# Kernel optimization log

Hardware: AMD Instinct MI355X
Metric: run time of the kernel (lower is better)

Reference implementation:

```python
import jax, jax.numpy as jnp
import numpy as np

N_EXPERTS = 8
TOP_K = 2


def setup_inputs() -> dict:
    key = jax.random.key(0)
    ks = jax.random.split(key, 5)
    B, T, D, E, H = 4, 2048, 1024, N_EXPERTS, 2730  # H = int(2*D*4/3)
    x = jax.random.normal(ks[0], (B, T, D), dtype=jnp.float32)
    gate_w = jax.random.normal(ks[1], (E, D), dtype=jnp.float32) * 0.02
    w1 = jax.random.normal(ks[2], (E, H, D), dtype=jnp.float32) * 0.02
    w3 = jax.random.normal(ks[3], (E, H, D), dtype=jnp.float32) * 0.02
    w2 = jax.random.normal(ks[4], (E, D, H), dtype=jnp.float32) * 0.02
    return {"x": x, "gate_w": gate_w, "w1": w1, "w3": w3, "w2": w2}


def reference(x, gate_w, w1, w3, w2):
    B, T, D = x.shape
    E = gate_w.shape[0]
    x_flat = x.reshape(-1, D)  # [N, D], N = B*T
    N = x_flat.shape[0]

    # Router: top-k over softmax probabilities, renormalized over selected experts
    logits = x_flat @ gate_w.T                      # [N, E]
    probs = jax.nn.softmax(logits, axis=-1)         # [N, E]
    top_v, top_i = jax.lax.top_k(probs, TOP_K)      # [N, K]
    top_v = top_v / jnp.sum(top_v, axis=-1, keepdims=True)

    # Dense combine weights [N, E]: weight of expert e for each token (0 if not selected).
    # top_k indices are distinct per token, so scatter-add equals scatter-set here.
    combine = jnp.zeros((N, E), dtype=x.dtype).at[
        jnp.arange(N)[:, None], top_i
    ].add(top_v)

    # Weighted combine of SwiGLU experts (loop over small fixed expert count).
    out = jnp.zeros_like(x_flat)
    for e in range(E):
        gate = jax.nn.silu(x_flat @ w1[e].T)        # [N, H]
        up = x_flat @ w3[e].T                       # [N, H]
        y = (gate * up) @ w2[e].T                   # [N, D]
        out = out + combine[:, e:e + 1] * y

    aux_loss = jnp.asarray(0.0, dtype=x.dtype)  # use_aux_loss=False / eval mode
    return out.reshape(B, T, D), aux_loss
```

## Files before the change

### kernel.cpp

```cpp
#include <hip/hip_runtime.h>
#include <hip/hip_bf16.h>

#define N_TOK 8192
#define D_DIM 1024
#define E_NUM 8
#define H_DIM 2730
#define HP    2816
#define NP    5632
#define NROWS (N_TOK*2)
#define MAXTILES 136
#define MAXT256  72

typedef __bf16 bf16;
typedef __bf16 bf16x8 __attribute__((ext_vector_type(8)));
typedef __bf16 bf16x4 __attribute__((ext_vector_type(4)));
typedef float  f32x4  __attribute__((ext_vector_type(4)));

__device__ __forceinline__ void gload_lds16(const bf16* g, bf16* l) {
  __builtin_amdgcn_global_load_lds((const __attribute__((address_space(1))) void*)g,
                                   (__attribute__((address_space(3))) void*)l, 16, 0, 0);
}
#define VMCNT(n) asm volatile("s_waitcnt vmcnt(" #n ")" ::: "memory")
#define LGKM0()  asm volatile("s_waitcnt lgkmcnt(0)" ::: "memory")
#define BAR() __builtin_amdgcn_s_barrier()

__global__ void conv13_kernel(const float* __restrict__ w1, const float* __restrict__ w3,
                              bf16* __restrict__ Bp) {
  int i = blockIdx.x * blockDim.x + threadIdx.x;
  if (i >= E_NUM * NP * 128) return;
  int c8 = i & 127;
  int r  = (i >> 7) % NP;
  int e  = i / (NP * 128);
  int hc = ((r >> 5) << 4) + (r & 15);
  bf16x8 o;
  if (hc < H_DIM) {
    const float* s = (((r >> 4) & 1) ? w3 : w1) + ((long)e * H_DIM + hc) * D_DIM + c8 * 8;
    float4 a0 = ((const float4*)s)[0], a1 = ((const float4*)s)[1];
    o[0]=(bf16)a0.x; o[1]=(bf16)a0.y; o[2]=(bf16)a0.z; o[3]=(bf16)a0.w;
    o[4]=(bf16)a1.x; o[5]=(bf16)a1.y; o[6]=(bf16)a1.z; o[7]=(bf16)a1.w;
  } else {
    #pragma unroll
    for (int j = 0; j < 8; j++) o[j] = (bf16)0.f;
  }
  ((bf16x8*)Bp)[i] = o;
}

__global__ void conv_w2_kernel(const float* __restrict__ src, bf16* __restrict__ dst) {
  int i = blockIdx.x * blockDim.x + threadIdx.x;
  if (i >= E_NUM * D_DIM * (HP / 8)) return;
  int c8 = i % (HP / 8);
  int row = i / (HP / 8);
  int c = c8 * 8;
  const float* s = src + (long)row * H_DIM + c;
  bf16x8 o;
  #pragma unroll
  for (int j = 0; j < 8; j++) o[j] = (c + j < H_DIM) ? (bf16)s[j] : (bf16)0.f;
  ((bf16x8*)dst)[i] = o;
}

__global__ void router_kernel(const float* __restrict__ x, const float* __restrict__ gw,
                              int* __restrict__ topi, float* __restrict__ topw,
                              int* __restrict__ counts) {
  int t = blockIdx.x * (blockDim.x >> 6) + (threadIdx.x >> 6);
  int lane = threadIdx.x & 63;
  if (t >= N_TOK) return;
  const float* xr = x + (long)t * D_DIM;
  float acc[E_NUM];
  #pragma unroll
  for (int e = 0; e < E_NUM; e++) acc[e] = 0.f;
  for (int j = 0; j < D_DIM / 64; j++) {
    float xv = xr[j * 64 + lane];
    #pragma unroll
    for (int e = 0; e < E_NUM; e++) acc[e] += xv * gw[e * D_DIM + j * 64 + lane];
  }
  #pragma unroll
  for (int e = 0; e < E_NUM; e++) {
    float v = acc[e];
    #pragma unroll
    for (int s = 32; s > 0; s >>= 1) v += __shfl_xor(v, s, 64);
    acc[e] = v;
  }
  if (lane == 0) {
    int b0 = -1, b1 = -1; float v0 = -1e30f, v1 = -1e30f;
    #pragma unroll
    for (int e = 0; e < E_NUM; e++) {
      float v = acc[e];
      if (v > v0) { v1 = v0; b1 = b0; v0 = v; b0 = e; }
      else if (v > v1) { v1 = v; b1 = e; }
    }
    float w0 = 1.f / (1.f + expf(v1 - v0));
    topi[t * 2] = b0; topi[t * 2 + 1] = b1;
    topw[t * 2] = w0; topw[t * 2 + 1] = 1.f - w0;
    atomicAdd(&counts[b0], 1); atomicAdd(&counts[b1], 1);
  }
}

__global__ void tiles_kernel(const int* __restrict__ counts, int* __restrict__ offs,
                             int* __restrict__ tlist, int* __restrict__ tlist2) {
  __shared__ int so[E_NUM + 1], sb[E_NUM + 1], sb2[E_NUM + 1];
  int t = threadIdx.x;
  if (t == 0) {
    int s = 0, b = 0, b2 = 0;
    for (int e = 0; e < E_NUM; e++) {
      so[e] = s; sb[e] = b; sb2[e] = b2;
      int ne = counts[e];
      s += ne; b += (ne + 127) >> 7; b2 += (ne + 255) >> 8;
    }
    so[E_NUM] = s; sb[E_NUM] = b; sb2[E_NUM] = b2;
  }
  __syncthreads();
  if (t <= E_NUM) offs[t] = so[t];
  for (int i = t; i < MAXTILES; i += blockDim.x) {
    int v = -1;
    #pragma unroll
    for (int e = 0; e < E_NUM; e++)
      if (i >= sb[e] && i < sb[e + 1]) v = (e << 8) | (i - sb[e]);
    tlist[i] = v;
  }
  for (int i = t; i < MAXT256; i += blockDim.x) {
    int v = -1;
    #pragma unroll
    for (int e = 0; e < E_NUM; e++)
      if (i >= sb2[e] && i < sb2[e + 1]) v = (e << 8) | (i - sb2[e]);
    tlist2[i] = v;
  }
}

__global__ void scatter_kernel(const int* __restrict__ topi, const float* __restrict__ topw,
                               const int* __restrict__ offs, int* __restrict__ cursor,
                               int* __restrict__ rowmap, float* __restrict__ roww,
                               int* __restrict__ rowoftok) {
  __shared__ int hist[E_NUM], base[E_NUM];
  int i = blockIdx.x * blockDim.x + threadIdx.x;
  if (threadIdx.x < E_NUM) hist[threadIdx.x] = 0;
  __syncthreads();
  int e = 0, lpos = 0;
  bool act = (i < NROWS);
  if (act) { e = topi[i]; lpos = atomicAdd(&hist[e], 1); }
  __syncthreads();
  if (threadIdx.x < E_NUM) base[threadIdx.x] = atomicAdd(&cursor[threadIdx.x], hist[threadIdx.x]);
  __syncthreads();
  if (act) {
    int row = offs[e] + base[e] + lpos;
    rowmap[row] = i >> 1;
    roww[row] = topw[i];
    rowoftok[i] = row;
  }
}

__global__ void gather_kernel(const float* __restrict__ x, const int* __restrict__ rowmap,
                              bf16* __restrict__ Xg) {
  int r = blockIdx.x * (blockDim.x >> 6) + (threadIdx.x >> 6);
  int lane = threadIdx.x & 63;
  if (r >= NROWS) return;
  int t = rowmap[r];
  const float4* src = (const float4*)(x + (long)t * D_DIM);
  bf16x4* dst = (bf16x4*)(Xg + (long)r * D_DIM);
  #pragma unroll
  for (int j = 0; j < 4; j++) {
    float4 v = src[j * 64 + lane];
    bf16x4 o; o[0]=(bf16)v.x; o[1]=(bf16)v.y; o[2]=(bf16)v.z; o[3]=(bf16)v.w;
    dst[j * 64 + lane] = o;
  }
}

__global__ void combine_kernel(const bf16* __restrict__ y0p, const bf16* __restrict__ y1p,
                               const int* __restrict__ rowoftok,
                               const float* __restrict__ topw, float* __restrict__ out) {
  int t = blockIdx.x * (blockDim.x >> 6) + (threadIdx.x >> 6);
  int lane = threadIdx.x & 63;
  if (t >= N_TOK) return;
  int r0 = rowoftok[t * 2], r1 = rowoftok[t * 2 + 1];
  float w0 = topw[t * 2], w1 = topw[t * 2 + 1];
  const bf16x8* a0 = (const bf16x8*)(y0p + (long)r0 * D_DIM);
  const bf16x8* a1 = (const bf16x8*)(y1p + (long)r0 * D_DIM);
  const bf16x8* b0 = (const bf16x8*)(y0p + (long)r1 * D_DIM);
  const bf16x8* b1 = (const bf16x8*)(y1p + (long)r1 * D_DIM);
  float* o = out + (long)t * D_DIM;
  #pragma unroll
  for (int j = 0; j < 2; j++) {
    int idx = j * 64 + lane;
    bf16x8 va0 = a0[idx], va1 = a1[idx], vb0 = b0[idx], vb1 = b1[idx];
    float4 v0, v1;
    v0.x = w0*((float)va0[0]+(float)va1[0]) + w1*((float)vb0[0]+(float)vb1[0]);
    v0.y = w0*((float)va0[1]+(float)va1[1]) + w1*((float)vb0[1]+(float)vb1[1]);
    v0.z = w0*((float)va0[2]+(float)va1[2]) + w1*((float)vb0[2]+(float)vb1[2]);
    v0.w = w0*((float)va0[3]+(float)va1[3]) + w1*((float)vb0[3]+(float)vb1[3]);
    v1.x = w0*((float)va0[4]+(float)va1[4]) + w1*((float)vb0[4]+(float)vb1[4]);
    v1.y = w0*((float)va0[5]+(float)va1[5]) + w1*((float)vb0[5]+(float)vb1[5]);
    v1.z = w0*((float)va0[6]+(float)va1[6]) + w1*((float)vb0[6]+(float)vb1[6]);
    v1.w = w0*((float)va0[7]+(float)va1[7]) + w1*((float)vb0[7]+(float)vb1[7]);
    float4* op = (float4*)(o + idx * 8);
    op[0] = v0; op[1] = v1;
  }
}


#define G1_STAGE(SB, T) do { \
    _Pragma("unroll") for (int L_ = 0; L_ < 4; L_++) \
      gload_lds16(aS[L_] + (T) * 32, smem + (SB) + w * 2048 + L_ * 512); \
    _Pragma("unroll") for (int L_ = 0; L_ < 2; L_++) \
      gload_lds16(bS[L_] + (T) * 32, smem + (SB) + 8192 + w * 1024 + L_ * 512); \
  } while (0)

#define G1_READ0(SB) do { \
    _Pragma("unroll") for (int m_ = 0; m_ < 4; m_++) \
      af[m_] = *(const bf16x8*)&smem[(SB) + (w * 64 + m_ * 16 + fr) * 32 + qp]; \
    _Pragma("unroll") for (int q_ = 0; q_ < 4; q_++) \
      bf0[q_] = *(const bf16x8*)&smem[(SB) + 8192 + (q_ * 16 + fr) * 32 + qp]; \
  } while (0)

#define G1_MFMA0() do { __builtin_amdgcn_s_setprio(1); \
    _Pragma("unroll") for (int m_ = 0; m_ < 4; m_++) \
    _Pragma("unroll") for (int q_ = 0; q_ < 4; q_++) \
      acc[m_][q_] = __builtin_amdgcn_mfma_f32_16x16x32_bf16(af[m_], bf0[q_], acc[m_][q_], 0, 0, 0); \
    __builtin_amdgcn_s_setprio(0); } while (0)

#define G1_READ1(SB) do { \
    _Pragma("unroll") for (int q_ = 0; q_ < 4; q_++) \
      bf1[q_] = *(const bf16x8*)&smem[(SB) + 8192 + ((q_ + 4) * 16 + fr) * 32 + qp]; \
  } while (0)

#define G1_MFMA1() do { __builtin_amdgcn_s_setprio(1); \
    _Pragma("unroll") for (int m_ = 0; m_ < 4; m_++) \
    _Pragma("unroll") for (int q_ = 0; q_ < 4; q_++) \
      acc[m_][q_ + 4] = __builtin_amdgcn_mfma_f32_16x16x32_bf16(af[m_], bf1[q_], acc[m_][q_ + 4], 0, 0, 0); \
    __builtin_amdgcn_s_setprio(0); } while (0)

__global__ __launch_bounds__(256, 2) void gemm1_kernel(
    const bf16* __restrict__ Xg, const bf16* __restrict__ Bp,
    const int* __restrict__ counts, const int* __restrict__ offs,
    const int* __restrict__ tlist2, bf16* __restrict__ h) {
  int bid = blockIdx.x;
  int tile = bid / 44, col = bid - tile * 44;
  int te = tlist2[tile];
  if (te < 0) return;
  int e = te >> 8, tm = te & 255;
  int ne = counts[e];
  int row_base = offs[e];
  int n0 = col * 128;

  __shared__ bf16 smem[3 * 12288];
  int tid = threadIdx.x, w = tid >> 6, lane = tid & 63;
  int fr = lane & 15, hi = lane >> 4;
  int qp = (hi ^ ((fr >> 1) & 3)) * 8;
  int srcq = ((lane & 3) ^ ((lane >> 3) & 3)) * 8;
  int srow = lane >> 2;

  f32x4 acc[4][8];
  #pragma unroll
  for (int m = 0; m < 4; m++)
    #pragma unroll
    for (int q = 0; q < 8; q++) acc[m][q] = (f32x4)0.f;

  const bf16* Bpe = Bp + (long)e * NP * D_DIM;
  const bf16* aS[4];
  const bf16* bS[2];
  #pragma unroll
  for (int L = 0; L < 4; L++) {
    int ra = row_base + min(tm * 256 + w * 64 + L * 16 + srow, ne - 1);
    aS[L] = Xg + (long)ra * D_DIM + srcq;
  }
  #pragma unroll
  for (int L = 0; L < 2; L++) {
    int rb = n0 + w * 32 + L * 16 + srow;
    bS[L] = Bpe + (long)rb * D_DIM + srcq;
  }

  bf16x8 af[4], bf0[4], bf1[4];

  G1_STAGE(0, 0); G1_STAGE(12288, 1);
  VMCNT(6); BAR();

  int sbC = 0, sbS = 24576;
  for (int t = 0; t < 30; t++) {
    G1_READ0(sbC);
    G1_STAGE(sbS, t + 2);
    BAR();
    G1_MFMA0();
    G1_READ1(sbC);
    G1_MFMA1();
    LGKM0(); VMCNT(6); BAR();
    sbC += 12288; if (sbC > 24576) sbC = 0;
    sbS += 12288; if (sbS > 24576) sbS = 0;
  }
  { G1_READ0(sbC); BAR(); G1_MFMA0(); G1_READ1(sbC); G1_MFMA1(); LGKM0(); VMCNT(0); BAR();
    sbC += 12288; if (sbC > 24576) sbC = 0; }
  { G1_READ0(sbC); G1_MFMA0(); G1_READ1(sbC); G1_MFMA1(); }

  int crow4 = hi * 4;
  #pragma unroll
  for (int m = 0; m < 4; m++)
    #pragma unroll
    for (int j = 0; j < 4; j++) {
      int rloc = tm * 256 + w * 64 + m * 16 + crow4 + j;
      if (rloc < ne) {
        long hrow = (long)(row_base + rloc) * HP;
        #pragma unroll
        for (int p = 0; p < 4; p++) {
          int col2 = (n0 >> 1) + p * 16 + fr;
          float g = acc[m][2 * p][j], u = acc[m][2 * p + 1][j];
          h[hrow + col2] = (bf16)((g / (1.f + __expf(-g))) * u);
        }
      }
    }
}

#define G2_STAGE(SB, T) do { \
    _Pragma("unroll") for (int L_ = 0; L_ < 2; L_++) \
      gload_lds16(aS[L_] + (T) * 32, smem2 + (SB) + w * 1024 + L_ * 512); \
    _Pragma("unroll") for (int L_ = 0; L_ < 4; L_++) \
      gload_lds16(bS[L_] + (T) * 32, smem2 + (SB) + 4096 + (L_ * 4 + w) * 512); \
  } while (0)

#define G2_READ0(SB) do { \
    _Pragma("unroll") for (int m_ = 0; m_ < 4; m_++) \
      af[m_] = *(const bf16x8*)&smem2[(SB) + (wr * 64 + m_ * 16 + fr) * 32 + qp]; \
    _Pragma("unroll") for (int n_ = 0; n_ < 4; n_++) \
      bf0[n_] = *(const bf16x8*)&smem2[(SB) + 4096 + (wc * 128 + n_ * 16 + fr) * 32 + qp]; \
  } while (0)

#define G2_MFMA0() do { __builtin_amdgcn_s_setprio(1); \
    _Pragma("unroll") for (int m_ = 0; m_ < 4; m_++) \
    _Pragma("unroll") for (int n_ = 0; n_ < 4; n_++) \
      acc[m_][n_] = __builtin_amdgcn_mfma_f32_16x16x32_bf16(af[m_], bf0[n_], acc[m_][n_], 0, 0, 0); \
    __builtin_amdgcn_s_setprio(0); } while (0)

#define G2_READ1(SB) do { \
    _Pragma("unroll") for (int n_ = 0; n_ < 4; n_++) \
      bf1[n_] = *(const bf16x8*)&smem2[(SB) + 4096 + (wc * 128 + (n_ + 4) * 16 + fr) * 32 + qp]; \
  } while (0)

#define G2_MFMA1() do { __builtin_amdgcn_s_setprio(1); \
    _Pragma("unroll") for (int m_ = 0; m_ < 4; m_++) \
    _Pragma("unroll") for (int n_ = 0; n_ < 4; n_++) \
      acc[m_][n_ + 4] = __builtin_amdgcn_mfma_f32_16x16x32_bf16(af[m_], bf1[n_], acc[m_][n_ + 4], 0, 0, 0); \
    __builtin_amdgcn_s_setprio(0); } while (0)

__global__ __launch_bounds__(256, 2) void gemm2_kernel(
    const bf16* __restrict__ h, const bf16* __restrict__ w2b,
    const int* __restrict__ counts, const int* __restrict__ offs,
    const int* __restrict__ tlist, bf16* __restrict__ y0p, bf16* __restrict__ y1p) {
  int bid = blockIdx.x;
  int tile = bid >> 3, col = (bid >> 1) & 3, ks = bid & 1;
  int te = tlist[tile];
  if (te < 0) return;
  int e = te >> 8, tm = te & 255;
  int ne = counts[e];
  int row_base = offs[e];
  int n0 = col * 256;
  int k0 = ks * 1408;

  __shared__ bf16 smem2[3 * 12288];
  int tid = threadIdx.x, w = tid >> 6, lane = tid & 63;
  int wr = w >> 1, wc = w & 1;
  int fr = lane & 15, hi = lane >> 4;
  int qp = (hi ^ ((fr >> 1) & 3)) * 8;
  int srcq = ((lane & 3) ^ ((lane >> 3) & 3)) * 8;
  int srow = lane >> 2;

  f32x4 acc[4][8];
  #pragma unroll
  for (int m = 0; m < 4; m++)
    #pragma unroll
    for (int n = 0; n < 8; n++) acc[m][n] = (f32x4)0.f;

  const bf16* w2e = w2b + (long)e * D_DIM * HP;
  const bf16* aS[2];
  const bf16* bS[4];
  #pragma unroll
  for (int L = 0; L < 2; L++) {
    int ra = row_base + min(tm * 128 + w * 32 + L * 16 + srow, ne - 1);
    aS[L] = h + (long)ra * HP + k0 + srcq;
  }
  #pragma unroll
  for (int L = 0; L < 4; L++) {
    int rb = n0 + (L * 4 + w) * 16 + srow;
    bS[L] = w2e + (long)rb * HP + k0 + srcq;
  }

  bf16x8 af[4], bf0[4], bf1[4];

  G2_STAGE(0, 0); G2_STAGE(12288, 1);
  VMCNT(6); BAR();

  int sbC = 0, sbS = 24576;
  for (int t = 0; t < 42; t++) {
    G2_READ0(sbC);
    G2_STAGE(sbS, t + 2);
    BAR();
    G2_MFMA0();
    G2_READ1(sbC);
    G2_MFMA1();
    LGKM0(); VMCNT(6); BAR();
    sbC += 12288; if (sbC > 24576) sbC = 0;
    sbS += 12288; if (sbS > 24576) sbS = 0;
  }
  { G2_READ0(sbC); BAR(); G2_MFMA0(); G2_READ1(sbC); G2_MFMA1(); LGKM0(); VMCNT(0); BAR();
    sbC += 12288; if (sbC > 24576) sbC = 0; }
  { G2_READ0(sbC); G2_MFMA0(); G2_READ1(sbC); G2_MFMA1(); }

  bf16* y = ks ? y1p : y0p;
  int crow4 = hi * 4;
  #pragma unroll
  for (int m = 0; m < 4; m++)
    #pragma unroll
    for (int j = 0; j < 4; j++) {
      int rloc = tm * 128 + wr * 64 + m * 16 + crow4 + j;
      if (rloc < ne) {
        long yrow = (long)(row_base + rloc) * D_DIM;
        #pragma unroll
        for (int n = 0; n < 8; n++) {
          int col2 = n0 + wc * 128 + n * 16 + fr;
          y[yrow + col2] = (bf16)acc[m][n][j];
        }
      }
    }
}

extern "C" void kernel_launch(void* const* d_in, const int* in_sizes, int n_in,
                              void* d_out, int out_size, void* d_ws, size_t ws_size,
                              hipStream_t stream) {
  const float* x  = (const float*)d_in[0];
  const float* gw = (const float*)d_in[1];
  const float* w1 = (const float*)d_in[2];
  const float* w3 = (const float*)d_in[3];
  const float* w2 = (const float*)d_in[4];
  float* out = (float*)d_out;

  char* ws = (char*)d_ws;
  int*   counts   = (int*)(ws);
  int*   cursor   = (int*)(ws + 64);
  int*   offs     = (int*)(ws + 128);
  int*   tlist    = (int*)(ws + 192);
  int*   tlist2   = (int*)(ws + 768);
  int*   topi     = (int*)(ws + 2048);
  float* topw     = (float*)(ws + 2048 + 65536);
  int*   rowmap   = (int*)(ws + 2048 + 131072);
  float* roww     = (float*)(ws + 2048 + 196608);
  int*   rowoftok = (int*)(ws + 2048 + 262144);
  char*  big      = ws + 2048 + 327680;
  bf16* Bp   = (bf16*)big;
  bf16* w2b  = (bf16*)big;
  bf16* y0   = (bf16*)(big + 46137344);
  bf16* Xg   = Bp + (size_t)E_NUM * NP * D_DIM;
  bf16* y1   = Xg;
  bf16* hbuf = Xg + (size_t)NROWS * D_DIM;

  hipMemsetAsync((char*)d_out + (size_t)(out_size - 1) * sizeof(float), 0, sizeof(float), stream);
  hipMemsetAsync(ws, 0, 256, stream);

  int nbp = E_NUM * NP * 128;
  conv13_kernel<<<(nbp + 255) / 256, 256, 0, stream>>>(w1, w3, Bp);

  router_kernel<<<N_TOK / 4, 256, 0, stream>>>(x, gw, topi, topw, counts);
  tiles_kernel<<<1, 192, 0, stream>>>(counts, offs, tlist, tlist2);
  scatter_kernel<<<(NROWS + 255) / 256, 256, 0, stream>>>(topi, topw, offs, cursor, rowmap, roww, rowoftok);
  gather_kernel<<<NROWS / 4, 256, 0, stream>>>(x, rowmap, Xg);

  gemm1_kernel<<<MAXT256 * 44, 256, 0, stream>>>(Xg, Bp, counts, offs, tlist2, hbuf);

  int w2n = E_NUM * D_DIM * (HP / 8);
  conv_w2_kernel<<<(w2n + 255) / 256, 256, 0, stream>>>(w2, w2b);

  gemm2_kernel<<<MAXTILES * 8, 256, 0, stream>>>(hbuf, w2b, counts, offs, tlist, y0, y1);
  combine_kernel<<<N_TOK / 4, 256, 0, stream>>>(y0, y1, rowoftok, topw, out);
}
```

Baseline: 654.1 us.

## Shrink gemm2 N-tile to 128 for more occupancy, interleave gemm1 tile pairs

```diff
diff --git a/kernel.cpp b/kernel.cpp
--- a/kernel.cpp
+++ b/kernel.cpp
@@ -232,7 +232,9 @@
     const int* __restrict__ counts, const int* __restrict__ offs,
     const int* __restrict__ tlist2, bf16* __restrict__ h) {
   int bid = blockIdx.x;
-  int tile = bid / 44, col = bid - tile * 44;
+  int pair = bid / 88, within = bid - pair * 88;
+  int col = within >> 1, tp = within & 1;
+  int tile = pair * 2 + tp;
   int te = tlist2[tile];
   if (te < 0) return;
   int e = te >> 8, tm = te & 255;
@@ -309,49 +311,38 @@
 #define G2_STAGE(SB, T) do { \
     _Pragma("unroll") for (int L_ = 0; L_ < 2; L_++) \
       gload_lds16(aS[L_] + (T) * 32, smem2 + (SB) + w * 1024 + L_ * 512); \
-    _Pragma("unroll") for (int L_ = 0; L_ < 4; L_++) \
-      gload_lds16(bS[L_] + (T) * 32, smem2 + (SB) + 4096 + (L_ * 4 + w) * 512); \
+    _Pragma("unroll") for (int L_ = 0; L_ < 2; L_++) \
+      gload_lds16(bS[L_] + (T) * 32, smem2 + (SB) + 4096 + w * 1024 + L_ * 512); \
   } while (0)
 
-#define G2_READ0(SB) do { \
+#define G2_READ(SB) do { \
     _Pragma("unroll") for (int m_ = 0; m_ < 4; m_++) \
       af[m_] = *(const bf16x8*)&smem2[(SB) + (wr * 64 + m_ * 16 + fr) * 32 + qp]; \
     _Pragma("unroll") for (int n_ = 0; n_ < 4; n_++) \
-      bf0[n_] = *(const bf16x8*)&smem2[(SB) + 4096 + (wc * 128 + n_ * 16 + fr) * 32 + qp]; \
+      bfr[n_] = *(const bf16x8*)&smem2[(SB) + 4096 + (wc * 64 + n_ * 16 + fr) * 32 + qp]; \
   } while (0)
 
-#define G2_MFMA0() do { __builtin_amdgcn_s_setprio(1); \
+#define G2_MFMA() do { __builtin_amdgcn_s_setprio(1); \
     _Pragma("unroll") for (int m_ = 0; m_ < 4; m_++) \
     _Pragma("unroll") for (int n_ = 0; n_ < 4; n_++) \
-      acc[m_][n_] = __builtin_amdgcn_mfma_f32_16x16x32_bf16(af[m_], bf0[n_], acc[m_][n_], 0, 0, 0); \
+      acc[m_][n_] = __builtin_amdgcn_mfma_f32_16x16x32_bf16(af[m_], bfr[n_], acc[m_][n_], 0, 0, 0); \
     __builtin_amdgcn_s_setprio(0); } while (0)
 
-#define G2_READ1(SB) do { \
-    _Pragma("unroll") for (int n_ = 0; n_ < 4; n_++) \
-      bf1[n_] = *(const bf16x8*)&smem2[(SB) + 4096 + (wc * 128 + (n_ + 4) * 16 + fr) * 32 + qp]; \
-  } while (0)
-
-#define G2_MFMA1() do { __builtin_amdgcn_s_setprio(1); \
-    _Pragma("unroll") for (int m_ = 0; m_ < 4; m_++) \
-    _Pragma("unroll") for (int n_ = 0; n_ < 4; n_++) \
-      acc[m_][n_ + 4] = __builtin_amdgcn_mfma_f32_16x16x32_bf16(af[m_], bf1[n_], acc[m_][n_ + 4], 0, 0, 0); \
-    __builtin_amdgcn_s_setprio(0); } while (0)
-
-__global__ __launch_bounds__(256, 2) void gemm2_kernel(
+__global__ __launch_bounds__(256, 3) void gemm2_kernel(
     const bf16* __restrict__ h, const bf16* __restrict__ w2b,
     const int* __restrict__ counts, const int* __restrict__ offs,
     const int* __restrict__ tlist, bf16* __restrict__ y0p, bf16* __restrict__ y1p) {
   int bid = blockIdx.x;
-  int tile = bid >> 3, col = (bid >> 1) & 3, ks = bid & 1;
+  int tile = bid >> 4, col = (bid >> 1) & 7, ks = bid & 1;
   int te = tlist[tile];
   if (te < 0) return;
   int e = te >> 8, tm = te & 255;
   int ne = counts[e];
   int row_base = offs[e];
-  int n0 = col * 256;
+  int n0 = col * 128;
   int k0 = ks * 1408;
 
-  __shared__ bf16 smem2[3 * 12288];
+  __shared__ bf16 smem2[3 * 8192];
   int tid = threadIdx.x, w = tid >> 6, lane = tid & 63;
   int wr = w >> 1, wc = w & 1;
   int fr = lane & 15, hi = lane >> 4;
@@ -359,46 +350,41 @@
   int srcq = ((lane & 3) ^ ((lane >> 3) & 3)) * 8;
   int srow = lane >> 2;
 
-  f32x4 acc[4][8];
+  f32x4 acc[4][4];
   #pragma unroll
   for (int m = 0; m < 4; m++)
     #pragma unroll
-    for (int n = 0; n < 8; n++) acc[m][n] = (f32x4)0.f;
+    for (int n = 0; n < 4; n++) acc[m][n] = (f32x4)0.f;
 
   const bf16* w2e = w2b + (long)e * D_DIM * HP;
   const bf16* aS[2];
-  const bf16* bS[4];
+  const bf16* bS[2];
   #pragma unroll
   for (int L = 0; L < 2; L++) {
     int ra = row_base + min(tm * 128 + w * 32 + L * 16 + srow, ne - 1);
     aS[L] = h + (long)ra * HP + k0 + srcq;
-  }
-  #pragma unroll
-  for (int L = 0; L < 4; L++) {
-    int rb = n0 + (L * 4 + w) * 16 + srow;
+    int rb = n0 + w * 32 + L * 16 + srow;
     bS[L] = w2e + (long)rb * HP + k0 + srcq;
   }
 
-  bf16x8 af[4], bf0[4], bf1[4];
-
-  G2_STAGE(0, 0); G2_STAGE(12288, 1);
-  VMCNT(6); BAR();
-
-  int sbC = 0, sbS = 24576;
+  bf16x8 af[4], bfr[4];
+
+  G2_STAGE(0, 0); G2_STAGE(8192, 1);
+  VMCNT(4); BAR();
+
+  int sbC = 0, sbS = 16384;
   for (int t = 0; t < 42; t++) {
-    G2_READ0(sbC);
+    G2_READ(sbC);
     G2_STAGE(sbS, t + 2);
     BAR();
-    G2_MFMA0();
-    G2_READ1(sbC);
-    G2_MFMA1();
-    LGKM0(); VMCNT(6); BAR();
-    sbC += 12288; if (sbC > 24576) sbC = 0;
-    sbS += 12288; if (sbS > 24576) sbS = 0;
-  }
-  { G2_READ0(sbC); BAR(); G2_MFMA0(); G2_READ1(sbC); G2_MFMA1(); LGKM0(); VMCNT(0); BAR();
-    sbC += 12288; if (sbC > 24576) sbC = 0; }
-  { G2_READ0(sbC); G2_MFMA0(); G2_READ1(sbC); G2_MFMA1(); }
+    G2_MFMA();
+    LGKM0(); VMCNT(4); BAR();
+    sbC += 8192; if (sbC > 16384) sbC = 0;
+    sbS += 8192; if (sbS > 16384) sbS = 0;
+  }
+  { G2_READ(sbC); BAR(); G2_MFMA(); LGKM0(); VMCNT(0); BAR();
+    sbC += 8192; if (sbC > 16384) sbC = 0; }
+  { G2_READ(sbC); G2_MFMA(); }
 
   bf16* y = ks ? y1p : y0p;
   int crow4 = hi * 4;
@@ -410,8 +396,8 @@
       if (rloc < ne) {
         long yrow = (long)(row_base + rloc) * D_DIM;
         #pragma unroll
-        for (int n = 0; n < 8; n++) {
-          int col2 = n0 + wc * 128 + n * 16 + fr;
+        for (int n = 0; n < 4; n++) {
+          int col2 = n0 + wc * 64 + n * 16 + fr;
           y[yrow + col2] = (bf16)acc[m][n][j];
         }
       }
@@ -463,6 +449,6 @@
   int w2n = E_NUM * D_DIM * (HP / 8);
   conv_w2_kernel<<<(w2n + 255) / 256, 256, 0, stream>>>(w2, w2b);
 
-  gemm2_kernel<<<MAXTILES * 8, 256, 0, stream>>>(hbuf, w2b, counts, offs, tlist, y0, y1);
+  gemm2_kernel<<<MAXTILES * 16, 256, 0, stream>>>(hbuf, w2b, counts, offs, tlist, y0, y1);
   combine_kernel<<<N_TOK / 4, 256, 0, stream>>>(y0, y1, rowoftok, topw, out);
 }
```

Result: no change. 659.8 us (+0.9%).
